# Kernel optimization log

Measured on AMD Instinct MI355X. Metric: run time of the kernel, lower is better.

Reference implementation:

```python
import jax, jax.numpy as jnp
import numpy as np
import math

B, T, C = 2, 2048, 2048
H, KV, HD = 16, 4, 128          # n_head, n_kv_head, head_dim
REP = H // KV
FFN = 5632                      # multiple_of-rounded 2/3 * 4 * n_embd
EPS = 1e-5


def setup_inputs() -> dict:
    key = jax.random.key(0)
    ks = jax.random.split(key, 10)
    s = 0.02
    x = jax.random.normal(ks[0], (B, T, C), dtype=jnp.float32)
    # RoPE table: (T, HD/2, 2) = (cos, sin)
    inv_freq = 1.0 / (10000.0 ** (np.arange(0, HD, 2, dtype=np.float32) / HD))
    ang = np.arange(T, dtype=np.float32)[:, None] * inv_freq[None, :]
    freqs_cis = jnp.asarray(np.stack([np.cos(ang), np.sin(ang)], axis=-1))
    wq = s * jax.random.normal(ks[1], (H * HD, C), dtype=jnp.float32)
    wk = s * jax.random.normal(ks[2], (KV * HD, C), dtype=jnp.float32)
    wv = s * jax.random.normal(ks[3], (KV * HD, C), dtype=jnp.float32)
    wo = s * jax.random.normal(ks[4], (C, H * HD), dtype=jnp.float32)
    w1 = s * jax.random.normal(ks[5], (FFN, C), dtype=jnp.float32)
    w2 = s * jax.random.normal(ks[6], (FFN, C), dtype=jnp.float32)
    c_proj = s * jax.random.normal(ks[7], (C, FFN), dtype=jnp.float32)
    g1 = jnp.ones((C,), dtype=jnp.float32)
    g2 = jnp.ones((C,), dtype=jnp.float32)
    return {"x": x, "freqs_cis": freqs_cis, "wq": wq, "wk": wk, "wv": wv,
            "wo": wo, "w1": w1, "w2": w2, "c_proj": c_proj, "g1": g1, "g2": g2}


def _rmsnorm(x, g, eps=EPS):
    return x * jax.lax.rsqrt(jnp.mean(x * x, axis=-1, keepdims=True) + eps) * g


def _rope(t, freqs_cis):
    # t: (B, T, nH, HD); freqs_cis: (T, HD/2, 2)
    tr = t.reshape(*t.shape[:-1], HD // 2, 2)
    cos = freqs_cis[None, :, None, :, 0]
    sin = freqs_cis[None, :, None, :, 1]
    out = jnp.stack([tr[..., 0] * cos - tr[..., 1] * sin,
                     tr[..., 0] * sin + tr[..., 1] * cos], axis=-1)
    return out.reshape(t.shape)


def reference(x, freqs_cis, wq, wk, wv, wo, w1, w2, c_proj, g1, g2):
    h = _rmsnorm(x, g1)
    q = (h @ wq.T).reshape(B, T, H, HD)
    k = (h @ wk.T).reshape(B, T, KV, HD)
    v = (h @ wv.T).reshape(B, T, KV, HD)
    q = _rope(q, freqs_cis)
    k = _rope(k, freqs_cis)
    # GQA: group query heads by kv head; never materialize expanded K/V
    q = q.transpose(0, 2, 1, 3).reshape(B, KV, REP, T, HD)  # b g r q d
    k = k.transpose(0, 2, 1, 3)                              # b g k d
    v = v.transpose(0, 2, 1, 3)                              # b g k d
    scale = 1.0 / math.sqrt(HD)
    scores = jnp.einsum('bgrqd,bgkd->bgrqk', q, k) * scale
    causal = jnp.tril(jnp.ones((T, T), dtype=bool))
    scores = jnp.where(causal, scores, jnp.float32(-1e30))
    attn = jax.nn.softmax(scores, axis=-1)
    y = jnp.einsum('bgrqk,bgkd->bgrqd', attn, v)
    y = y.reshape(B, H, T, HD).transpose(0, 2, 1, 3).reshape(B, T, C)
    x = x + y @ wo.T
    h2 = _rmsnorm(x, g2)
    mlp = (jax.nn.silu(h2 @ w1.T) * (h2 @ w2.T)) @ c_proj.T
    return x + mlp
```

## Files before the change

### kernel.cpp

```cpp
#include <hip/hip_runtime.h>
#include <hip/hip_bf16.h>
#include <math.h>

#define TT   2048
#define CC   2048
#define NB   2
#define NH   16
#define NKV  4
#define HDIM 128
#define NFFN 5632

typedef __attribute__((ext_vector_type(8))) short     bf8;
typedef __attribute__((ext_vector_type(4))) float     f32x4;
typedef __attribute__((ext_vector_type(8))) unsigned short u16x8;
typedef __attribute__((ext_vector_type(4))) unsigned short u16x4;

__device__ __forceinline__ float b2f(unsigned short u) {
    union { unsigned u; float f; } v; v.u = ((unsigned)u) << 16; return v.f;
}
__device__ __forceinline__ unsigned short f2bf(float f) {
    union { float f; unsigned u; } v; v.f = f;
    unsigned r = (v.u + 0x7fffu + ((v.u >> 16) & 1u)) >> 16;
    return (unsigned short)r;
}
__device__ __forceinline__ void gll16(const void* g, void* l) {
    __builtin_amdgcn_global_load_lds((const __attribute__((address_space(1))) void*)g,
                                     (__attribute__((address_space(3))) void*)l, 16, 0, 0);
}

__global__ __launch_bounds__(256) void cvt_k(const float* __restrict__ in,
        __hip_bfloat16* __restrict__ out)
{
    const size_t i = ((size_t)blockIdx.x * 256 + threadIdx.x) * 8;
    float4 a = *(const float4*)(in + i);
    float4 b = *(const float4*)(in + i + 4);
    u16x8 v;
    v[0] = f2bf(a.x); v[1] = f2bf(a.y); v[2] = f2bf(a.z); v[3] = f2bf(a.w);
    v[4] = f2bf(b.x); v[5] = f2bf(b.y); v[6] = f2bf(b.z); v[7] = f2bf(b.w);
    *(u16x8*)((unsigned short*)out + i) = v;
}

__global__ __launch_bounds__(256) void rms_f32_k(const float* __restrict__ x,
        const float* __restrict__ g, __hip_bfloat16* __restrict__ o)
{
    const size_t row = blockIdx.x;
    const int e0 = threadIdx.x * 8;
    float4 a = *(const float4*)(x + row * CC + e0);
    float4 b = *(const float4*)(x + row * CC + e0 + 4);
    float vals[8] = {a.x, a.y, a.z, a.w, b.x, b.y, b.z, b.w};
    float s = 0.f;
    #pragma unroll
    for (int e = 0; e < 8; ++e) s += vals[e] * vals[e];
    #pragma unroll
    for (int off = 32; off; off >>= 1) s += __shfl_xor(s, off);
    __shared__ float wsum[4];
    if ((threadIdx.x & 63) == 0) wsum[threadIdx.x >> 6] = s;
    __syncthreads();
    float scale = rsqrtf((wsum[0] + wsum[1] + wsum[2] + wsum[3]) * (1.0f / CC) + 1e-5f);
    float4 g0 = *(const float4*)(g + e0);
    float4 g1 = *(const float4*)(g + e0 + 4);
    float gs[8] = {g0.x, g0.y, g0.z, g0.w, g1.x, g1.y, g1.z, g1.w};
    u16x8 ov;
    #pragma unroll
    for (int e = 0; e < 8; ++e) ov[e] = f2bf(vals[e] * scale * gs[e]);
    *(u16x8*)((unsigned short*)o + row * CC + e0) = ov;
}

__global__ __launch_bounds__(256) void rms_bf16_k(const __hip_bfloat16* __restrict__ x,
        const float* __restrict__ g, __hip_bfloat16* __restrict__ o)
{
    const size_t row = blockIdx.x;
    const int e0 = threadIdx.x * 8;
    u16x8 xv = *(const u16x8*)((const unsigned short*)x + row * CC + e0);
    float vals[8];
    #pragma unroll
    for (int e = 0; e < 8; ++e) vals[e] = b2f(xv[e]);
    float s = 0.f;
    #pragma unroll
    for (int e = 0; e < 8; ++e) s += vals[e] * vals[e];
    #pragma unroll
    for (int off = 32; off; off >>= 1) s += __shfl_xor(s, off);
    __shared__ float wsum[4];
    if ((threadIdx.x & 63) == 0) wsum[threadIdx.x >> 6] = s;
    __syncthreads();
    float scale = rsqrtf((wsum[0] + wsum[1] + wsum[2] + wsum[3]) * (1.0f / CC) + 1e-5f);
    float4 g0 = *(const float4*)(g + e0);
    float4 g1 = *(const float4*)(g + e0 + 4);
    float gs[8] = {g0.x, g0.y, g0.z, g0.w, g1.x, g1.y, g1.z, g1.w};
    u16x8 ov;
    #pragma unroll
    for (int e = 0; e < 8; ++e) ov[e] = f2bf(vals[e] * scale * gs[e]);
    *(u16x8*)((unsigned short*)o + row * CC + e0) = ov;
}

#define GBM 128
#define GBN 128
#define GBK 32

template<int EPI, int OUTB>
__global__ __launch_bounds__(256) void gemm_db(
        const __hip_bfloat16* __restrict__ A,
        const __hip_bfloat16* __restrict__ W,
        const void* __restrict__ Rp,
        void* __restrict__ Cp,
        int M, int N, int K)
{
    __shared__ alignas(16) __hip_bfloat16 As[2][GBM][GBK];
    __shared__ alignas(16) __hip_bfloat16 Ws[2][GBN][GBK];
    const int tid  = threadIdx.x;
    const int lane = tid & 63;
    const int wid  = tid >> 6;
    const int wr = wid >> 1, wc = wid & 1;
    const int nwg = gridDim.x * gridDim.y;
    const int lin = blockIdx.y * gridDim.x + blockIdx.x;
    const int nlin = (lin & 7) * (nwg >> 3) + (lin >> 3);
    const int bxs = nlin % gridDim.x, bys = nlin / gridDim.x;
    const int bm = bys * GBM, bn = bxs * GBN;
    const int l4  = lane >> 2;
    const int lk8 = (lane & 3) * 8;
    const int fr  = lane & 15;
    const int fk  = (lane >> 4) * 8;

    f32x4 acc[4][4];
    #pragma unroll
    for (int m = 0; m < 4; ++m)
        #pragma unroll
        for (int n = 0; n < 4; ++n) acc[m][n] = (f32x4){0.f, 0.f, 0.f, 0.f};

    const __hip_bfloat16* ga0 = A + (size_t)(bm + wid * 32 + l4) * K + lk8;
    const __hip_bfloat16* ga1 = A + (size_t)(bm + wid * 32 + 16 + l4) * K + lk8;
    const __hip_bfloat16* gw0 = W + (size_t)(bn + wid * 32 + l4) * K + lk8;
    const __hip_bfloat16* gw1 = W + (size_t)(bn + wid * 32 + 16 + l4) * K + lk8;

    const int nt = K >> 5;
    gll16(ga0, &As[0][wid * 32][0]);
    gll16(ga1, &As[0][wid * 32 + 16][0]);
    gll16(gw0, &Ws[0][wid * 32][0]);
    gll16(gw1, &Ws[0][wid * 32 + 16][0]);

    #pragma unroll 2
    for (int t = 0; t < nt; ++t) {
        const int cur = t & 1;
        __syncthreads();
        if (t + 1 < nt) {
            const int k1 = (t + 1) << 5;
            const int nx = cur ^ 1;
            gll16(ga0 + k1, &As[nx][wid * 32][0]);
            gll16(ga1 + k1, &As[nx][wid * 32 + 16][0]);
            gll16(gw0 + k1, &Ws[nx][wid * 32][0]);
            gll16(gw1 + k1, &Ws[nx][wid * 32 + 16][0]);
        }
        bf8 af[4];
        #pragma unroll
        for (int m = 0; m < 4; ++m)
            af[m] = *(const bf8*)&As[cur][wr * 64 + m * 16 + fr][fk];
        #pragma unroll
        for (int n = 0; n < 4; ++n) {
            bf8 wf = *(const bf8*)&Ws[cur][wc * 64 + n * 16 + fr][fk];
            #pragma unroll
            for (int m = 0; m < 4; ++m)
                acc[m][n] = __builtin_amdgcn_mfma_f32_16x16x32_bf16(af[m], wf, acc[m][n], 0, 0, 0);
        }
    }

    const int rj = (lane >> 4) * 4;
    #pragma unroll
    for (int m = 0; m < 4; ++m) {
        #pragma unroll
        for (int j = 0; j < 4; ++j) {
            const size_t row = (size_t)(bm + wr * 64 + m * 16 + rj + j);
            #pragma unroll
            for (int n = 0; n < 4; ++n) {
                const size_t col = (size_t)(bn + wc * 64 + n * 16 + fr);
                float v = acc[m][n][j];
                if (EPI == 1) v += ((const float*)Rp)[row * N + col];
                if (EPI == 2) v += b2f(((const unsigned short*)Rp)[row * N + col]);
                if (EPI == 3) {
                    float gv = b2f(((const unsigned short*)Rp)[row * N + col]);
                    v = (gv / (1.0f + __expf(-gv))) * v;
                }
                if (OUTB) ((unsigned short*)Cp)[row * N + col] = f2bf(v);
                else      ((float*)Cp)[row * N + col] = v;
            }
        }
    }
}

__global__ __launch_bounds__(256) void gemm_qkv_db(
        const __hip_bfloat16* __restrict__ A,
        const __hip_bfloat16* __restrict__ W,
        const float* __restrict__ fc,
        __hip_bfloat16* __restrict__ qo,
        __hip_bfloat16* __restrict__ ko,
        __hip_bfloat16* __restrict__ vto,
        int M, int K)
{
    __shared__ alignas(16) __hip_bfloat16 As[2][GBM][GBK];
    __shared__ alignas(16) __hip_bfloat16 Ws[2][GBN][GBK];
    const int tid  = threadIdx.x;
    const int lane = tid & 63;
    const int wid  = tid >> 6;
    const int wr = wid >> 1, wc = wid & 1;
    const int nwg = gridDim.x * gridDim.y;
    const int lin = blockIdx.y * gridDim.x + blockIdx.x;
    const int nlin = (lin & 7) * (nwg >> 3) + (lin >> 3);
    const int bxs = nlin % gridDim.x, bys = nlin / gridDim.x;
    const int bm = bys * GBM, bn = bxs * GBN;
    const int l4  = lane >> 2;
    const int lk8 = (lane & 3) * 8;
    const int fr  = lane & 15;
    const int fk  = (lane >> 4) * 8;

    f32x4 acc[4][4];
    #pragma unroll
    for (int m = 0; m < 4; ++m)
        #pragma unroll
        for (int n = 0; n < 4; ++n) acc[m][n] = (f32x4){0.f, 0.f, 0.f, 0.f};

    const __hip_bfloat16* ga0 = A + (size_t)(bm + wid * 32 + l4) * K + lk8;
    const __hip_bfloat16* ga1 = A + (size_t)(bm + wid * 32 + 16 + l4) * K + lk8;
    const __hip_bfloat16* gw0 = W + (size_t)(bn + wid * 32 + l4) * K + lk8;
    const __hip_bfloat16* gw1 = W + (size_t)(bn + wid * 32 + 16 + l4) * K + lk8;

    const int nt = K >> 5;
    gll16(ga0, &As[0][wid * 32][0]);
    gll16(ga1, &As[0][wid * 32 + 16][0]);
    gll16(gw0, &Ws[0][wid * 32][0]);
    gll16(gw1, &Ws[0][wid * 32 + 16][0]);

    #pragma unroll 2
    for (int t = 0; t < nt; ++t) {
        const int cur = t & 1;
        __syncthreads();
        if (t + 1 < nt) {
            const int k1 = (t + 1) << 5;
            const int nx = cur ^ 1;
            gll16(ga0 + k1, &As[nx][wid * 32][0]);
            gll16(ga1 + k1, &As[nx][wid * 32 + 16][0]);
            gll16(gw0 + k1, &Ws[nx][wid * 32][0]);
            gll16(gw1 + k1, &Ws[nx][wid * 32 + 16][0]);
        }
        bf8 af[4];
        #pragma unroll
        for (int m = 0; m < 4; ++m)
            af[m] = *(const bf8*)&As[cur][wr * 64 + m * 16 + fr][fk];
        #pragma unroll
        for (int n = 0; n < 4; ++n) {
            bf8 wf = *(const bf8*)&Ws[cur][wc * 64 + n * 16 + fr][fk];
            #pragma unroll
            for (int m = 0; m < 4; ++m)
                acc[m][n] = __builtin_amdgcn_mfma_f32_16x16x32_bf16(af[m], wf, acc[m][n], 0, 0, 0);
        }
    }

    const int rj = (lane >> 4) * 4;
    #pragma unroll
    for (int m = 0; m < 4; ++m) {
        #pragma unroll
        for (int n = 0; n < 4; ++n) {
            const int col = bn + wc * 64 + n * 16 + fr;
            const int row0 = bm + wr * 64 + m * 16 + rj;
            if (col < 2560) {
                const int i2 = ((col & 127) >> 1) * 2;
                const int role = col & 1;
                #pragma unroll
                for (int j = 0; j < 4; ++j) {
                    const int t0 = (row0 + j) & (TT - 1);
                    const float cv = fc[t0 * HDIM + i2];
                    const float sv = fc[t0 * HDIM + i2 + 1];
                    const float v = acc[m][n][j];
                    const float partner = __shfl_xor(v, 1);
                    const float o = role ? (partner * sv + v * cv) : (v * cv - partner * sv);
                    if (col < 2048)
                        ((unsigned short*)qo)[(size_t)(row0 + j) * CC + col] = f2bf(o);
                    else
                        ((unsigned short*)ko)[(size_t)(row0 + j) * (NKV * HDIM) + (col - 2048)] = f2bf(o);
                }
            } else {
                const int vc = col - 2560;
                const int g = vc >> 7, d = vc & 127;
                const int b = row0 >> 11, t0 = row0 & (TT - 1);
                unsigned short* vp = (unsigned short*)vto +
                    ((size_t)(b * NKV + g) * HDIM + d) * TT + t0;
                u16x4 ov;
                #pragma unroll
                for (int j = 0; j < 4; ++j) ov[j] = f2bf(acc[m][n][j]);
                *(u16x4*)vp = ov;
            }
        }
    }
}

#define PBM 128
#define PBN 256
#define PBK 64

template<int EPI, int OUTB>
__global__ __launch_bounds__(512) void gemm_8p(
        const __hip_bfloat16* __restrict__ A,
        const __hip_bfloat16* __restrict__ W,
        const void* __restrict__ Rp,
        void* __restrict__ Cp,
        int M, int N, int K)
{
    __shared__ alignas(16) __hip_bfloat16 As[2][PBM][PBK];
    __shared__ alignas(16) __hip_bfloat16 Ws[2][PBN][PBK];
    const int tid  = threadIdx.x;
    const int lane = tid & 63;
    const int wid  = tid >> 6;
    const int wr = wid >> 2, wc = wid & 3;
    const int nwg = gridDim.x * gridDim.y;
    const int lin = blockIdx.y * gridDim.x + blockIdx.x;
    const int nlin = (lin & 7) * (nwg >> 3) + (lin >> 3);
    const int bxs = nlin % gridDim.x, bys = nlin / gridDim.x;
    const int bm = bys * PBM, bn = bxs * PBN;
    const int fr = lane & 15;
    const int hi = lane >> 4;

    f32x4 acc[4][4];
    #pragma unroll
    for (int m = 0; m < 4; ++m)
        #pragma unroll
        for (int n = 0; n < 4; ++n) acc[m][n] = (f32x4){0.f, 0.f, 0.f, 0.f};

    const unsigned short* Ag = (const unsigned short*)A;
    const unsigned short* Wg = (const unsigned short*)W;

    auto STAGE = [&](int buf, int k0) {
        #pragma unroll
        for (int l = 0; l < 2; ++l) {
            const int s = l * 512 + tid;
            const int row = s >> 3;
            const int srcb = ((s & 7) * 16) ^ ((row & 7) << 4);
            gll16(Ag + (size_t)(bm + row) * K + k0 + (srcb >> 1),
                  (unsigned short*)&As[buf][0][0] + (l * 512 + wid * 64) * 8);
        }
        #pragma unroll
        for (int l = 0; l < 4; ++l) {
            const int s = l * 512 + tid;
            const int row = s >> 3;
            const int srcb = ((s & 7) * 16) ^ ((row & 7) << 4);
            gll16(Wg + (size_t)(bn + row) * K + k0 + (srcb >> 1),
                  (unsigned short*)&Ws[buf][0][0] + (l * 512 + wid * 64) * 8);
        }
    };

    const int nt = K >> 6;
    STAGE(0, 0);
    __syncthreads();

    for (int t = 0; t < nt; ++t) {
        const int cur = t & 1;
        const char* Ab = (const char*)&As[cur][0][0];
        const char* Bb = (const char*)&Ws[cur][0][0];

        bf8 bF[4][2];
        #pragma unroll
        for (int n = 0; n < 4; ++n) {
            const int row = wc * 64 + n * 16 + fr;
            #pragma unroll
            for (int kk = 0; kk < 2; ++kk) {
                const int off = (kk * 64 + hi * 16) ^ ((row & 7) << 4);
                bF[n][kk] = *(const bf8*)(Bb + row * 128 + off);
            }
        }
        bf8 a0, a1;
        {
            const int row = wr * 64 + fr;
            a0 = *(const bf8*)(Ab + row * 128 + ((hi * 16)      ^ ((row & 7) << 4)));
            a1 = *(const bf8*)(Ab + row * 128 + ((64 + hi * 16) ^ ((row & 7) << 4)));
        }
        if (t + 1 < nt) STAGE(cur ^ 1, (t + 1) * PBK);
        __builtin_amdgcn_s_barrier();
        __builtin_amdgcn_s_setprio(1);
        #pragma unroll
        for (int n = 0; n < 4; ++n) {
            acc[0][n] = __builtin_amdgcn_mfma_f32_16x16x32_bf16(a0, bF[n][0], acc[0][n], 0, 0, 0);
            acc[0][n] = __builtin_amdgcn_mfma_f32_16x16x32_bf16(a1, bF[n][1], acc[0][n], 0, 0, 0);
        }
        __builtin_amdgcn_s_setprio(0);
        __builtin_amdgcn_s_barrier();

        #pragma unroll
        for (int m = 1; m < 4; ++m) {
            const int row = wr * 64 + m * 16 + fr;
            bf8 am0 = *(const bf8*)(Ab + row * 128 + ((hi * 16)      ^ ((row & 7) << 4)));
            bf8 am1 = *(const bf8*)(Ab + row * 128 + ((64 + hi * 16) ^ ((row & 7) << 4)));
            __builtin_amdgcn_s_barrier();
            __builtin_amdgcn_s_setprio(1);
            #pragma unroll
            for (int n = 0; n < 4; ++n) {
                acc[m][n] = __builtin_amdgcn_mfma_f32_16x16x32_bf16(am0, bF[n][0], acc[m][n], 0, 0, 0);
                acc[m][n] = __builtin_amdgcn_mfma_f32_16x16x32_bf16(am1, bF[n][1], acc[m][n], 0, 0, 0);
            }
            __builtin_amdgcn_s_setprio(0);
            if (m < 3) __builtin_amdgcn_s_barrier();
        }
        __syncthreads();
    }

    const int rj = hi * 4;
    #pragma unroll
    for (int m = 0; m < 4; ++m) {
        #pragma unroll
        for (int j = 0; j < 4; ++j) {
            const size_t row = (size_t)(bm + wr * 64 + m * 16 + rj + j);
            #pragma unroll
            for (int n = 0; n < 4; ++n) {
                const size_t col = (size_t)(bn + wc * 64 + n * 16 + fr);
                float v = acc[m][n][j];
                if (EPI == 1) v += ((const float*)Rp)[row * N + col];
                if (EPI == 2) v += b2f(((const unsigned short*)Rp)[row * N + col]);
                if (EPI == 3) {
                    float gv = b2f(((const unsigned short*)Rp)[row * N + col]);
                    v = (gv / (1.0f + __expf(-gv))) * v;
                }
                if (OUTB) ((unsigned short*)Cp)[row * N + col] = f2bf(v);
                else      ((float*)Cp)[row * N + col] = v;
            }
        }
    }
}

#define AQB 128
#define AKV 64

__global__ __launch_bounds__(512) void attn_mfma(const __hip_bfloat16* __restrict__ q,
        const __hip_bfloat16* __restrict__ k, const __hip_bfloat16* __restrict__ vt,
        __hip_bfloat16* __restrict__ y)
{
    __shared__ alignas(16) unsigned short Ks[2][AKV * HDIM];
    __shared__ alignas(16) unsigned short Vs[2][HDIM * AKV];
    __shared__ alignas(16) unsigned short Ps[AQB * AKV];

    const int qt = (TT / AQB - 1) - blockIdx.x;
    const int h  = blockIdx.y;
    const int b  = blockIdx.z;
    const int g  = h >> 2;
    const int qbase = qt * AQB;

    const int tid  = threadIdx.x;
    const int lane = tid & 63;
    const int wid  = tid >> 6;
    const int fr   = lane & 15;
    const int fk8  = (lane >> 4) * 8;
    const int rj   = (lane >> 4) * 4;

    bf8 qf[4];
    {
        const unsigned short* qp = (const unsigned short*)q +
            (size_t)(b * TT + qbase + wid * 16 + fr) * CC + h * HDIM;
        #pragma unroll
        for (int c = 0; c < 4; ++c)
            qf[c] = *(const bf8*)(qp + c * 32 + fk8);
    }
    const unsigned short* vtb = (const unsigned short*)vt + (size_t)(b * NKV + g) * HDIM * TT;

    f32x4 oacc[8];
    float m_r[4], l_r[4];
    #pragma unroll
    for (int n = 0; n < 8; ++n) oacc[n] = (f32x4){0.f, 0.f, 0.f, 0.f};
    #pragma unroll
    for (int j = 0; j < 4; ++j) { m_r[j] = -1e30f; l_r[j] = 0.f; }

    const float scale = 0.08838834764831845f;
    const int ntiles = qbase / AKV + 2;
    const int kjr = tid >> 3;
    const int kkc = (tid & 7) * 16;
    const int vdr = tid >> 2;
    const int vjc = (tid & 3) * 16;

    u16x8 krg[2], vrg[2];
    auto LOADT = [&](int jb) {
        const unsigned short* kp = (const unsigned short*)k +
            ((size_t)(b * TT + jb + kjr) * (NKV * HDIM)) + g * HDIM + kkc;
        const unsigned short* vp = vtb + (size_t)vdr * TT + jb + vjc;
        #pragma unroll
        for (int c = 0; c < 2; ++c) {
            krg[c] = *(const u16x8*)(kp + c * 8);
            vrg[c] = *(const u16x8*)(vp + c * 8);
        }
    };
    auto WRITET = [&](int buf) {
        #pragma unroll
        for (int c = 0; c < 2; ++c) {
            const int byteK = (kjr * 256 + (kkc + c * 8) * 2) ^ ((kjr & 7) << 4);
            *(u16x8*)((char*)&Ks[buf][0] + byteK) = krg[c];
            const int byteV = (vdr * 128 + (vjc + c * 8) * 2) ^ ((vdr & 7) << 4);
            *(u16x8*)((char*)&Vs[buf][0] + byteV) = vrg[c];
        }
    };

    LOADT(0);
    WRITET(0);

    for (int tile = 0; tile < ntiles; ++tile) {
        const int cur = tile & 1;
        if (tile + 1 < ntiles) LOADT((tile + 1) * AKV);
        __syncthreads();

        f32x4 s[4];
        #pragma unroll
        for (int n = 0; n < 4; ++n) s[n] = (f32x4){0.f, 0.f, 0.f, 0.f};
        __builtin_amdgcn_s_setprio(1);
        #pragma unroll
        for (int c = 0; c < 4; ++c) {
            #pragma unroll
            for (int n = 0; n < 4; ++n) {
                const int j = n * 16 + fr;
                const int byteB = (j * 256 + (c * 32 + fk8) * 2) ^ ((j & 7) << 4);
                bf8 kf = *(const bf8*)((char*)&Ks[cur][0] + byteB);
                s[n] = __builtin_amdgcn_mfma_f32_16x16x32_bf16(qf[c], kf, s[n], 0, 0, 0);
            }
        }
        __builtin_amdgcn_s_setprio(0);

        const int jbase = tile * AKV;
        #pragma unroll
        for (int jj = 0; jj < 4; ++jj) {
            const int qg = qbase + wid * 16 + rj + jj;
            float sv[4];
            #pragma unroll
            for (int n = 0; n < 4; ++n) {
                const int jg = jbase + n * 16 + fr;
                sv[n] = (jg <= qg) ? s[n][jj] * scale : -1e30f;
            }
            float tmax = fmaxf(fmaxf(sv[0], sv[1]), fmaxf(sv[2], sv[3]));
            tmax = fmaxf(tmax, __shfl_xor(tmax, 1));
            tmax = fmaxf(tmax, __shfl_xor(tmax, 2));
            tmax = fmaxf(tmax, __shfl_xor(tmax, 4));
            tmax = fmaxf(tmax, __shfl_xor(tmax, 8));
            const float mnew = fmaxf(m_r[jj], tmax);
            const float alpha = __expf(m_r[jj] - mnew);
            m_r[jj] = mnew;
            const int prow = wid * 16 + rj + jj;
            float tsum = 0.f;
            #pragma unroll
            for (int n = 0; n < 4; ++n) {
                const float p = __expf(sv[n] - mnew);
                tsum += p;
                const int byteP = (prow * 128 + (n * 16 + fr) * 2) ^ ((prow & 7) << 4);
                *(unsigned short*)((char*)Ps + byteP) = f2bf(p);
            }
            tsum += __shfl_xor(tsum, 1);
            tsum += __shfl_xor(tsum, 2);
            tsum += __shfl_xor(tsum, 4);
            tsum += __shfl_xor(tsum, 8);
            l_r[jj] = l_r[jj] * alpha + tsum;
            #pragma unroll
            for (int n = 0; n < 8; ++n) oacc[n][jj] *= alpha;
        }

        __builtin_amdgcn_s_setprio(1);
        #pragma unroll
        for (int c2 = 0; c2 < 2; ++c2) {
            const int prow = wid * 16 + fr;
            const int byteA = (prow * 128 + (c2 * 32 + fk8) * 2) ^ ((prow & 7) << 4);
            bf8 pf = *(const bf8*)((char*)Ps + byteA);
            #pragma unroll
            for (int n = 0; n < 8; ++n) {
                const int d = n * 16 + fr;
                const int byteB = (d * 128 + (c2 * 32 + fk8) * 2) ^ ((d & 7) << 4);
                bf8 vf = *(const bf8*)((char*)&Vs[cur][0] + byteB);
                oacc[n] = __builtin_amdgcn_mfma_f32_16x16x32_bf16(pf, vf, oacc[n], 0, 0, 0);
            }
        }
        __builtin_amdgcn_s_setprio(0);

        if (tile + 1 < ntiles) WRITET(cur ^ 1);
    }

    #pragma unroll
    for (int jj = 0; jj < 4; ++jj) {
        const float inv = 1.0f / l_r[jj];
        unsigned short* yrow = (unsigned short*)y +
            ((size_t)(b * TT + qbase + wid * 16 + rj + jj) * CC) + h * HDIM;
        #pragma unroll
        for (int n = 0; n < 8; ++n)
            yrow[n * 16 + fr] = f2bf(oacc[n][jj] * inv);
    }
}

extern "C" void kernel_launch(void* const* d_in, const int* in_sizes, int n_in,
                              void* d_out, int out_size, void* d_ws, size_t ws_size,
                              hipStream_t stream)
{
    (void)in_sizes; (void)n_in; (void)out_size; (void)ws_size;
    const float* x     = (const float*)d_in[0];
    const float* fc    = (const float*)d_in[1];
    const float* wq    = (const float*)d_in[2];
    const float* wk    = (const float*)d_in[3];
    const float* wv    = (const float*)d_in[4];
    const float* wo    = (const float*)d_in[5];
    const float* w1    = (const float*)d_in[6];
    const float* w2    = (const float*)d_in[7];
    const float* cproj = (const float*)d_in[8];
    const float* g1    = (const float*)d_in[9];
    const float* g2    = (const float*)d_in[10];
    float* out = (float*)d_out;

    const int ROWS = NB * TT;
    unsigned char* wsb = (unsigned char*)d_ws;
    __hip_bfloat16* x2b = (__hip_bfloat16*)(wsb);
    __hip_bfloat16* hb  = (__hip_bfloat16*)(wsb + 16777216u);
    __hip_bfloat16* w1b = (__hip_bfloat16*)(wsb + 33554432u);
    __hip_bfloat16* w2b = (__hip_bfloat16*)(wsb + 56623104u);
    __hip_bfloat16* G1  = (__hip_bfloat16*)(wsb + 79691776u);
    __hip_bfloat16* cpb = w1b;
    __hip_bfloat16* qb   = (__hip_bfloat16*)(wsb + 33554432u);
    __hip_bfloat16* kb   = (__hip_bfloat16*)(wsb + 50331648u);
    __hip_bfloat16* vtb  = (__hip_bfloat16*)(wsb + 54525952u);
    __hip_bfloat16* yb   = (__hip_bfloat16*)(wsb + 58720256u);
    __hip_bfloat16* wbuf = (__hip_bfloat16*)(wsb + 75497472u);

    rms_f32_k<<<ROWS, 256, 0, stream>>>(x, g1, hb);
    cvt_k<<<(CC * CC) / 2048, 256, 0, stream>>>(wq, wbuf);
    cvt_k<<<(NKV * HDIM * CC) / 2048, 256, 0, stream>>>(wk, wbuf + (size_t)2048 * CC);
    cvt_k<<<(NKV * HDIM * CC) / 2048, 256, 0, stream>>>(wv, wbuf + (size_t)2560 * CC);
    gemm_qkv_db<<<dim3(3072 / GBN, ROWS / GBM), 256, 0, stream>>>(hb, wbuf, fc, qb, kb, vtb, ROWS, CC);
    attn_mfma<<<dim3(TT / AQB, NH, NB), 512, 0, stream>>>(qb, kb, vtb, yb);
    cvt_k<<<(CC * CC) / 2048, 256, 0, stream>>>(wo, wbuf);
    gemm_db<1, 1><<<dim3(CC / GBN, ROWS / GBM), 256, 0, stream>>>(yb, wbuf, x, x2b, ROWS, CC, CC);
    rms_bf16_k<<<ROWS, 256, 0, stream>>>(x2b, g2, hb);
    cvt_k<<<(NFFN * CC) / 2048, 256, 0, stream>>>(w1, w1b);
    cvt_k<<<(NFFN * CC) / 2048, 256, 0, stream>>>(w2, w2b);
    gemm_8p<0, 1><<<dim3(NFFN / PBN, ROWS / PBM), 512, 0, stream>>>(hb, w1b, nullptr, G1, ROWS, NFFN, CC);
    gemm_8p<3, 1><<<dim3(NFFN / PBN, ROWS / PBM), 512, 0, stream>>>(hb, w2b, G1, G1, ROWS, NFFN, CC);
    cvt_k<<<(CC * NFFN) / 2048, 256, 0, stream>>>(cproj, cpb);
    gemm_8p<2, 0><<<dim3(CC / PBN, ROWS / PBM), 512, 0, stream>>>(G1, cpb, x2b, out, ROWS, CC, NFFN);
}
```

Measured before the change: 675.4 us.

## Split attention KV range in two with combine pass; use 8-wave GEMM for output projection

Each query tile's causal KV range is split into two halves processed by separate blocks, which write unnormalised bf16 partial outputs plus per-row max and sum. A new combine kernel merges the two halves with log-sum-exp rescaling and writes the normalised result. This doubles the attention grid, giving more parallelism and better load balance across the causal triangle, at the cost of extra global traffic and one more launch. The output projection also moves from gemm_db to the 512-thread gemm_8p kernel.

Result: no change. 684.6 us (+1.4%).

```diff
diff --git a/kernel.cpp b/kernel.cpp
--- a/kernel.cpp
+++ b/kernel.cpp
@@ -425,19 +425,21 @@
 #define AQB 128
 #define AKV 64
 
-__global__ __launch_bounds__(512) void attn_mfma(const __hip_bfloat16* __restrict__ q,
+__global__ __launch_bounds__(512) void attn_part(const __hip_bfloat16* __restrict__ q,
         const __hip_bfloat16* __restrict__ k, const __hip_bfloat16* __restrict__ vt,
-        __hip_bfloat16* __restrict__ y)
+        __hip_bfloat16* __restrict__ Opart, float* __restrict__ ML)
 {
     __shared__ alignas(16) unsigned short Ks[2][AKV * HDIM];
     __shared__ alignas(16) unsigned short Vs[2][HDIM * AKV];
     __shared__ alignas(16) unsigned short Ps[AQB * AKV];
 
-    const int qt = (TT / AQB - 1) - blockIdx.x;
+    const int pt = blockIdx.x & 1;
+    const int qt = (TT / AQB - 1) - (blockIdx.x >> 1);
     const int h  = blockIdx.y;
     const int b  = blockIdx.z;
     const int g  = h >> 2;
     const int qbase = qt * AQB;
+    const int bh = b * NH + h;
 
     const int tid  = threadIdx.x;
     const int lane = tid & 63;
@@ -461,10 +463,12 @@
     #pragma unroll
     for (int n = 0; n < 8; ++n) oacc[n] = (f32x4){0.f, 0.f, 0.f, 0.f};
     #pragma unroll
-    for (int j = 0; j < 4; ++j) { m_r[j] = -1e30f; l_r[j] = 0.f; }
+    for (int j = 0; j < 4; ++j) { m_r[j] = -30000.0f; l_r[j] = 0.f; }
 
     const float scale = 0.08838834764831845f;
-    const int ntiles = qbase / AKV + 2;
+    const int half = (qbase >> 6) / 2 + 1;
+    const int tbeg = pt * half;
+    const int tend = tbeg + half;
     const int kjr = tid >> 3;
     const int kkc = (tid & 7) * 16;
     const int vdr = tid >> 2;
@@ -491,12 +495,12 @@
         }
     };
 
-    LOADT(0);
+    LOADT(tbeg * AKV);
     WRITET(0);
 
-    for (int tile = 0; tile < ntiles; ++tile) {
-        const int cur = tile & 1;
-        if (tile + 1 < ntiles) LOADT((tile + 1) * AKV);
+    for (int tile = tbeg; tile < tend; ++tile) {
+        const int cur = (tile - tbeg) & 1;
+        if (tile + 1 < tend) LOADT((tile + 1) * AKV);
         __syncthreads();
 
         f32x4 s[4];
@@ -567,18 +571,52 @@
         }
         __builtin_amdgcn_s_setprio(0);
 
-        if (tile + 1 < ntiles) WRITET(cur ^ 1);
-    }
-
+        if (tile + 1 < tend) WRITET(cur ^ 1);
+    }
+
+    unsigned short* Ob = (unsigned short*)Opart + (size_t)pt * NB * NH * TT * HDIM;
+    float* MLb = ML + (size_t)pt * NB * NH * TT * 2;
     #pragma unroll
     for (int jj = 0; jj < 4; ++jj) {
-        const float inv = 1.0f / l_r[jj];
-        unsigned short* yrow = (unsigned short*)y +
-            ((size_t)(b * TT + qbase + wid * 16 + rj + jj) * CC) + h * HDIM;
+        const int grow = qbase + wid * 16 + rj + jj;
+        unsigned short* orow = Ob + ((size_t)bh * TT + grow) * HDIM;
         #pragma unroll
         for (int n = 0; n < 8; ++n)
-            yrow[n * 16 + fr] = f2bf(oacc[n][jj] * inv);
-    }
+            orow[n * 16 + fr] = f2bf(oacc[n][jj]);
+        if (fr == 0) {
+            float* mlp = MLb + ((size_t)bh * TT + grow) * 2;
+            mlp[0] = m_r[jj];
+            mlp[1] = l_r[jj];
+        }
+    }
+}
+
+__global__ __launch_bounds__(256) void attn_combine(
+        const __hip_bfloat16* __restrict__ Opart, const float* __restrict__ ML,
+        __hip_bfloat16* __restrict__ y)
+{
+    const int unit = blockIdx.x * 16 + (threadIdx.x >> 4);
+    const int d8 = (threadIdx.x & 15) * 8;
+    const int bh = unit >> 11;
+    const int grow = unit & (TT - 1);
+    const int b = bh >> 4, h = bh & 15;
+    const size_t ri = (size_t)bh * TT + grow;
+    const float* ml0 = ML + ri * 2;
+    const float* ml1 = ML + (size_t)NB * NH * TT * 2 + ri * 2;
+    const float m0 = ml0[0], l0 = ml0[1];
+    const float m1 = ml1[0], l1 = ml1[1];
+    const float m = fmaxf(m0, m1);
+    const float e0 = __expf(m0 - m), e1 = __expf(m1 - m);
+    const float inv = 1.0f / (l0 * e0 + l1 * e1);
+    const unsigned short* p0 = (const unsigned short*)Opart + ri * HDIM + d8;
+    const unsigned short* p1 = (const unsigned short*)Opart + (size_t)NB * NH * TT * HDIM + ri * HDIM + d8;
+    u16x8 a = *(const u16x8*)p0;
+    u16x8 c = *(const u16x8*)p1;
+    u16x8 o;
+    #pragma unroll
+    for (int e = 0; e < 8; ++e)
+        o[e] = f2bf((b2f(a[e]) * e0 + b2f(c[e]) * e1) * inv);
+    *(u16x8*)((unsigned short*)y + ((size_t)(b * TT + grow) * CC) + h * HDIM + d8) = o;
 }
 
 extern "C" void kernel_launch(void* const* d_in, const int* in_sizes, int n_in,
@@ -612,15 +650,18 @@
     __hip_bfloat16* vtb  = (__hip_bfloat16*)(wsb + 54525952u);
     __hip_bfloat16* yb   = (__hip_bfloat16*)(wsb + 58720256u);
     __hip_bfloat16* wbuf = (__hip_bfloat16*)(wsb + 75497472u);
+    __hip_bfloat16* Opart = (__hip_bfloat16*)(wsb + 92274688u);
+    float* MLbuf = (float*)(wsb);
 
     rms_f32_k<<<ROWS, 256, 0, stream>>>(x, g1, hb);
     cvt_k<<<(CC * CC) / 2048, 256, 0, stream>>>(wq, wbuf);
     cvt_k<<<(NKV * HDIM * CC) / 2048, 256, 0, stream>>>(wk, wbuf + (size_t)2048 * CC);
     cvt_k<<<(NKV * HDIM * CC) / 2048, 256, 0, stream>>>(wv, wbuf + (size_t)2560 * CC);
     gemm_qkv_db<<<dim3(3072 / GBN, ROWS / GBM), 256, 0, stream>>>(hb, wbuf, fc, qb, kb, vtb, ROWS, CC);
-    attn_mfma<<<dim3(TT / AQB, NH, NB), 512, 0, stream>>>(qb, kb, vtb, yb);
+    attn_part<<<dim3((TT / AQB) * 2, NH, NB), 512, 0, stream>>>(qb, kb, vtb, Opart, MLbuf);
+    attn_combine<<<(NB * NH * TT) / 16, 256, 0, stream>>>(Opart, MLbuf, yb);
     cvt_k<<<(CC * CC) / 2048, 256, 0, stream>>>(wo, wbuf);
-    gemm_db<1, 1><<<dim3(CC / GBN, ROWS / GBM), 256, 0, stream>>>(yb, wbuf, x, x2b, ROWS, CC, CC);
+    gemm_8p<1, 1><<<dim3(CC / PBN, ROWS / PBM), 512, 0, stream>>>(yb, wbuf, x, x2b, ROWS, CC, CC);
     rms_bf16_k<<<ROWS, 256, 0, stream>>>(x2b, g2, hb);
     cvt_k<<<(NFFN * CC) / 2048, 256, 0, stream>>>(w1, w1b);
     cvt_k<<<(NFFN * CC) / 2048, 256, 0, stream>>>(w2, w2b);
```
